# Kernel tuning notes

Measured on AMD Instinct MI355X. Metric: run time of the kernel, lower is better.

## Reference

```python
import jax, jax.numpy as jnp
import numpy as np

B, N = 32, 262144

def setup_inputs() -> dict:
    key = jax.random.key(0)
    k1, k2, k3, k4, k5 = jax.random.split(key, 5)
    F_mat = jax.random.normal(k1, (B, 3, 3), jnp.float32)
    f = 800.0 + 50.0 * jax.random.normal(k2, (B,), jnp.float32)
    K = (jnp.zeros((B, 3, 3), jnp.float32)
         .at[:, 0, 0].set(f).at[:, 1, 1].set(f)
         .at[:, 0, 2].set(320.0).at[:, 1, 2].set(240.0)
         .at[:, 2, 2].set(1.0))
    pts1_flat = jax.random.uniform(k3, (N, 2), jnp.float32) * 640.0
    pts2_flat = jax.random.uniform(k4, (N, 2), jnp.float32) * 640.0
    batch_indices = jnp.sort(jax.random.randint(k5, (N,), 0, B))
    return {"F_mat": F_mat, "K": K, "pts1_flat": pts1_flat,
            "pts2_flat": pts2_flat, "batch_indices": batch_indices}

def _pose_candidates(E):
    # torch.svd returns V (not V^T); the original code uses R = U @ W @ V.
    U, S, Vh = jnp.linalg.svd(E)
    U = U * jnp.where(jnp.linalg.det(U) < 0, -1.0, 1.0)[:, None, None]
    Vh = Vh * jnp.where(jnp.linalg.det(Vh) < 0, -1.0, 1.0)[:, None, None]
    V = jnp.swapaxes(Vh, -1, -2)  # = torch's "Vt" variable (which is V)
    W = jnp.array([[0.0, -1.0, 0.0], [1.0, 0.0, 0.0], [0.0, 0.0, 1.0]], E.dtype)
    R1 = U @ W @ V
    R2 = U @ W.T @ V
    t = U[:, :, 2]
    R_cand = jnp.stack([R1, R1, R2, R2], axis=1)          # [B,4,3,3]
    t_cand = jnp.stack([t, -t, t, -t], axis=1)            # [B,4,3]
    return R_cand, t_cand

def _cheirality_scores(R_cand, t_cand, K, pts1_flat, pts2_flat, batch_indices):
    n = pts1_flat.shape[0]
    Kinv = jnp.linalg.inv(K)[batch_indices]               # [N,3,3]
    ones = jnp.ones((n, 1), pts1_flat.dtype)
    p1 = jnp.einsum('nij,nj->ni', Kinv, jnp.concatenate([pts1_flat, ones], 1))[:, :2]
    p2 = jnp.einsum('nij,nj->ni', Kinv, jnp.concatenate([pts2_flat, ones], 1))[:, :2]
    P2 = jnp.concatenate([R_cand, t_cand[..., None]], axis=-1)  # [B,4,3,4]
    P2n = P2[batch_indices]                                     # [N,4,3,4]
    # A rows for P1 = [I|0]: A0 = [-1,0,x1,0], A1 = [0,-1,y1,0]
    z = jnp.zeros((n,), p1.dtype)
    A0 = jnp.stack([-jnp.ones_like(z), z, p1[:, 0], z], axis=-1)  # [N,4]
    A1 = jnp.stack([z, -jnp.ones_like(z), p1[:, 1], z], axis=-1)
    A2 = p2[:, 0, None, None] * P2n[:, :, 2, :] - P2n[:, :, 0, :]  # [N,4,4]
    A3 = p2[:, 1, None, None] * P2n[:, :, 2, :] - P2n[:, :, 1, :]
    A = jnp.stack([jnp.broadcast_to(A0[:, None, :], A2.shape),
                   jnp.broadcast_to(A1[:, None, :], A2.shape), A2, A3], axis=2)  # [N,4,4,4]
    _, _, Vh = jnp.linalg.svd(A)
    vec = Vh[..., :, -1]                      # = last ROW of V, faithful to torch code
    pts3d = vec[..., :3] / vec[..., 3:4]      # [N,4,3]
    z1 = pts3d[..., 2]                        # depth in cam 1 (P1 = [I|0])
    z2 = jnp.sum(P2n[:, :, 2, :3] * pts3d, axis=-1) + P2n[:, :, 2, 3]
    in_front = ((z1 > 0) & (z2 > 0)).astype(jnp.float32)  # [N,4]
    scores = jax.ops.segment_sum(in_front, batch_indices, num_segments=B)  # [B,4]
    counts = jax.ops.segment_sum(jnp.ones((n,), jnp.float32), batch_indices, num_segments=B)
    return scores, counts

def reference(F_mat, K, pts1_flat, pts2_flat, batch_indices):
    E = jnp.einsum('bji,bjk,bkl->bil', K, F_mat, K)       # K^T F K
    R_cand, t_cand = _pose_candidates(E)
    scores, counts = _cheirality_scores(R_cand, t_cand, K, pts1_flat, pts2_flat, batch_indices)
    best_idx = jnp.argmax(scores, axis=1)                 # first max, like torch '>'
    has = (counts > 0).astype(R_cand.dtype)
    bi = jnp.arange(B)
    best_R = R_cand[bi, best_idx] * has[:, None, None]
    best_t = t_cand[bi, best_idx] * has[:, None]
    best_candidate = jnp.where(counts > 0, best_idx, 0)
    return best_R, best_t, best_candidate
```

## Files before the change

### kernel.cpp

```cpp
#include <hip/hip_runtime.h>
#include <math.h>


#define NBATCH 32
#define USE_NEW_SLARTG 1

#define EPS4  5.9604645e-08f
#define UNFL4 1.1754944e-38f
#define TOL4  (10.0f * EPS4)


__device__ __forceinline__ float sign_f(float a, float b) {
  return (b >= 0.0f) ? fabsf(a) : -fabsf(a);
}

__device__ __forceinline__ float slapy2f(float x, float y) {
#pragma clang fp contract(off)
  float xa = fabsf(x), ya = fabsf(y);
  float w = fmaxf(xa, ya), z = fminf(xa, ya);
  if (z == 0.0f) return w;
  float r = z / w;
  return w * sqrtf(1.0f + r * r);
}

__device__ __forceinline__ void slartg_(float f, float g, float* cs, float* sn, float* r) {
#pragma clang fp contract(off)
#if USE_NEW_SLARTG
  if (g == 0.0f) { *cs = 1.0f; *sn = 0.0f; *r = f; return; }
  if (f == 0.0f) { *cs = 0.0f; *sn = (g >= 0.0f) ? 1.0f : -1.0f; *r = fabsf(g); return; }
  float d = sqrtf(f * f + g * g);
  *cs = fabsf(f) / d;
  float rr = (f >= 0.0f) ? d : -d;
  *sn = g / rr;
  *r = rr;
#else
  if (g == 0.0f) { *cs = 1.0f; *sn = 0.0f; *r = f; return; }
  if (f == 0.0f) { *cs = 0.0f; *sn = 1.0f; *r = g; return; }
  float rr = sqrtf(f * f + g * g);
  float c = f / rr, s = g / rr;
  if (fabsf(f) > fabsf(g) && c < 0.0f) { c = -c; s = -s; rr = -rr; }
  *cs = c; *sn = s; *r = rr;
#endif
}

__device__ __forceinline__ void slas2_(float f, float g, float h, float* ssmin, float* ssmax) {
#pragma clang fp contract(off)
  float fa = fabsf(f), ga = fabsf(g), ha = fabsf(h);
  float fhmn = fminf(fa, ha), fhmx = fmaxf(fa, ha);
  if (fhmn == 0.0f) {
    *ssmin = 0.0f;
    if (fhmx == 0.0f) { *ssmax = ga; }
    else {
      float mx = fmaxf(fhmx, ga), mn = fminf(fhmx, ga);
      float r = mn / mx;
      *ssmax = mx * sqrtf(1.0f + r * r);
    }
  } else {
    if (ga < fhmx) {
      float as_ = 1.0f + fhmn / fhmx;
      float at = (fhmx - fhmn) / fhmx;
      float au = ga / fhmx; au = au * au;
      float c = 2.0f / (sqrtf(as_ * as_ + au) + sqrtf(at * at + au));
      *ssmin = fhmn * c;
      *ssmax = fhmx / c;
    } else {
      float au = fhmx / ga;
      if (au == 0.0f) { *ssmin = (fhmn * fhmx) / ga; *ssmax = ga; }
      else {
        float as_ = 1.0f + fhmn / fhmx;
        float at = (fhmx - fhmn) / fhmx;
        float aas = as_ * au, aat = at * au;
        float c = 1.0f / (sqrtf(1.0f + aas * aas) + sqrtf(1.0f + aat * aat));
        float sm = (fhmn * c) * au;
        *ssmin = sm + sm;
        *ssmax = ga / (c + c);
      }
    }
  }
}

__device__ __forceinline__ void slasv2_(float f, float g, float h, float* ssmin, float* ssmax,
                        float* snr, float* csr, float* snl, float* csl) {
#pragma clang fp contract(off)
  const float EPS = EPS4;
  float ft = f, fa = fabsf(f), ht = h, ha = fabsf(h);
  int pmax = 1;
  bool swap_ = (ha > fa);
  if (swap_) {
    pmax = 3;
    float t = ft; ft = ht; ht = t;
    t = fa; fa = ha; ha = t;
  }
  float gt = g, ga = fabsf(g);
  float clt = 0.f, crt = 0.f, slt = 0.f, srt = 0.f;
  if (ga == 0.0f) {
    *ssmin = ha; *ssmax = fa;
    clt = 1.0f; crt = 1.0f; slt = 0.0f; srt = 0.0f;
  } else {
    bool gasmal = true;
    if (ga > fa) {
      pmax = 2;
      if ((fa / ga) < EPS) {
        gasmal = false;
        *ssmax = ga;
        if (ha > 1.0f) *ssmin = fa / (ga / ha);
        else *ssmin = (fa / ga) * ha;
        clt = 1.0f; slt = ht / gt; srt = 1.0f; crt = ft / gt;
      }
    }
    if (gasmal) {
      float dd = fa - ha;
      float l;
      if (dd == fa) l = 1.0f; else l = dd / fa;
      float mm_ = gt / ft;
      float t = 2.0f - l;
      float mm = mm_ * mm_, tt = t * t;
      float s = sqrtf(tt + mm);
      float r;
      if (l == 0.0f) r = fabsf(mm_); else r = sqrtf(l * l + mm);
      float a = 0.5f * (s + r);
      *ssmin = ha / a;
      *ssmax = fa * a;
      if (mm == 0.0f) {
        if (l == 0.0f) t = sign_f(2.0f, ft) * sign_f(1.0f, gt);
        else t = gt / sign_f(dd, ft) + mm_ / t;
      } else {
        t = (mm_ / (s + t) + mm_ / (r + l)) * (1.0f + a);
      }
      float l2 = sqrtf(t * t + 4.0f);
      crt = 2.0f / l2;
      srt = t / l2;
      clt = (crt + srt * mm_) / a;
      slt = (ht / ft) * srt / a;
    }
  }
  if (swap_) { *csl = srt; *snl = crt; *csr = slt; *snr = clt; }
  else { *csl = clt; *snl = slt; *csr = crt; *snr = srt; }
  float tsign = 1.0f;
  if (pmax == 1) tsign = sign_f(1.0f, *csr) * sign_f(1.0f, *csl) * sign_f(1.0f, f);
  if (pmax == 2) tsign = sign_f(1.0f, *snr) * sign_f(1.0f, *csl) * sign_f(1.0f, g);
  if (pmax == 3) tsign = sign_f(1.0f, *snr) * sign_f(1.0f, *snl) * sign_f(1.0f, h);
  *ssmax = sign_f(*ssmax, tsign);
  *ssmin = sign_f(*ssmin, tsign * sign_f(1.0f, f) * sign_f(1.0f, h));
}


__device__ __forceinline__ void sv3_chase(float (&d)[3], float (&e)[2],
                                          float (&vt)[3][3], float (&u)[3][3],
                                          float thresh, int& iter, int& oldll,
                                          int& oldm, int& idir, float smax) {
#pragma clang fp contract(off)
  if (1 > oldm || 3 < oldll)
    idir = (fabsf(d[0]) >= fabsf(d[2])) ? 1 : 2;

  bool deflated = false;
  float sminl = 0.0f;
  if (idir == 1) {
    if (fabsf(e[1]) <= TOL4 * fabsf(d[2])) { e[1] = 0.0f; return; }
    float mu = fabsf(d[0]); sminl = mu;
    if (fabsf(e[0]) <= TOL4 * mu) { e[0] = 0.0f; deflated = true; }
    else {
      mu = fabsf(d[1]) * (mu / (mu + fabsf(e[0])));
      if (mu < sminl) sminl = mu;
      if (fabsf(e[1]) <= TOL4 * mu) { e[1] = 0.0f; deflated = true; }
      else {
        mu = fabsf(d[2]) * (mu / (mu + fabsf(e[1])));
        if (mu < sminl) sminl = mu;
      }
    }
  } else {
    if (fabsf(e[0]) <= TOL4 * fabsf(d[0])) { e[0] = 0.0f; return; }
    float mu = fabsf(d[2]); sminl = mu;
    if (fabsf(e[1]) <= TOL4 * mu) { e[1] = 0.0f; deflated = true; }
    else {
      mu = fabsf(d[1]) * (mu / (mu + fabsf(e[1])));
      if (mu < sminl) sminl = mu;
      if (fabsf(e[0]) <= TOL4 * mu) { e[0] = 0.0f; deflated = true; }
      else {
        mu = fabsf(d[0]) * (mu / (mu + fabsf(e[0])));
        if (mu < sminl) sminl = mu;
      }
    }
  }
  if (deflated) return;
  oldll = 1; oldm = 3;

  float shift = 0.0f, rdum;
  if (!(3.0f * TOL4 * (sminl / smax) <= fmaxf(EPS4, 0.01f * TOL4))) {
    float sll;
    if (idir == 1) { sll = fabsf(d[0]); slas2_(d[1], e[1], d[2], &shift, &rdum); }
    else { sll = fabsf(d[2]); slas2_(d[0], e[0], d[1], &shift, &rdum); }
    if (sll > 0.0f) {
      float q = shift / sll;
      if (q * q < EPS4) shift = 0.0f;
    }
  }
  iter += 2;

  if (shift == 0.0f) {
    if (idir == 1) {
      float cs = 1.0f, oldcs = 1.0f, sn = 0.0f, oldsn = 0.0f, r = 0.0f;
      float c1, s1, c2, s2, rr;
      slartg_(d[0] * cs, e[0], &c1, &s1, &r); cs = c1; sn = s1;
      slartg_(oldcs * r, d[1] * sn, &c2, &s2, &rr); oldcs = c2; oldsn = s2;
      d[0] = rr;
#pragma unroll
      for (int k = 0; k < 3; k++) {
        float x = vt[0][k], y = vt[1][k];
        vt[0][k] = cs * x + sn * y; vt[1][k] = cs * y - sn * x;
      }
#pragma unroll
      for (int k = 0; k < 3; k++) {
        float x = u[k][0], y = u[k][1];
        u[k][0] = oldcs * x + oldsn * y; u[k][1] = oldcs * y - oldsn * x;
      }
      slartg_(d[1] * cs, e[1], &c1, &s1, &r); cs = c1; sn = s1;
      e[0] = oldsn * r;
      slartg_(oldcs * r, d[2] * sn, &c2, &s2, &rr); oldcs = c2; oldsn = s2;
      d[1] = rr;
#pragma unroll
      for (int k = 0; k < 3; k++) {
        float x = vt[1][k], y = vt[2][k];
        vt[1][k] = cs * x + sn * y; vt[2][k] = cs * y - sn * x;
      }
#pragma unroll
      for (int k = 0; k < 3; k++) {
        float x = u[k][1], y = u[k][2];
        u[k][1] = oldcs * x + oldsn * y; u[k][2] = oldcs * y - oldsn * x;
      }
      float h = d[2] * cs;
      d[2] = h * oldcs;
      e[1] = h * oldsn;
      if (fabsf(e[1]) <= thresh) e[1] = 0.0f;
    } else {
      float cs = 1.0f, oldcs = 1.0f, sn = 0.0f, oldsn = 0.0f, r = 0.0f;
      float c1, s1, c2, s2, rr;
      slartg_(d[2] * cs, e[1], &c1, &s1, &r); cs = c1; sn = s1;
      slartg_(oldcs * r, d[1] * sn, &c2, &s2, &rr); oldcs = c2; oldsn = s2;
      d[2] = rr;
#pragma unroll
      for (int k = 0; k < 3; k++) {
        float x = u[k][2], y = u[k][1];
        u[k][2] = cs * x + sn * y; u[k][1] = cs * y - sn * x;
      }
#pragma unroll
      for (int k = 0; k < 3; k++) {
        float x = vt[2][k], y = vt[1][k];
        vt[2][k] = oldcs * x + oldsn * y; vt[1][k] = oldcs * y - oldsn * x;
      }
      slartg_(d[1] * cs, e[0], &c1, &s1, &r); cs = c1; sn = s1;
      e[1] = oldsn * r;
      slartg_(oldcs * r, d[0] * sn, &c2, &s2, &rr); oldcs = c2; oldsn = s2;
      d[1] = rr;
#pragma unroll
      for (int k = 0; k < 3; k++) {
        float x = u[k][1], y = u[k][0];
        u[k][1] = cs * x + sn * y; u[k][0] = cs * y - sn * x;
      }
#pragma unroll
      for (int k = 0; k < 3; k++) {
        float x = vt[1][k], y = vt[0][k];
        vt[1][k] = oldcs * x + oldsn * y; vt[0][k] = oldcs * y - oldsn * x;
      }
      float h = d[0] * cs;
      d[0] = h * oldcs;
      e[0] = h * oldsn;
      if (fabsf(e[0]) <= thresh) e[0] = 0.0f;
    }
  } else {
    if (idir == 1) {
      float f = (fabsf(d[0]) - shift) * (sign_f(1.0f, d[0]) + shift / d[0]);
      float g = e[0];
      float cosr, sinr, cosl, sinl, r, rr;
      slartg_(f, g, &cosr, &sinr, &r);
      f = cosr * d[0] + sinr * e[0];
      e[0] = cosr * e[0] - sinr * d[0];
      g = sinr * d[1];
      d[1] = cosr * d[1];
      slartg_(f, g, &cosl, &sinl, &rr);
      d[0] = rr;
      f = cosl * e[0] + sinl * d[1];
      d[1] = cosl * d[1] - sinl * e[0];
      g = sinl * e[1];
      e[1] = cosl * e[1];
#pragma unroll
      for (int k = 0; k < 3; k++) {
        float x = vt[0][k], y = vt[1][k];
        vt[0][k] = cosr * x + sinr * y; vt[1][k] = cosr * y - sinr * x;
      }
#pragma unroll
      for (int k = 0; k < 3; k++) {
        float x = u[k][0], y = u[k][1];
        u[k][0] = cosl * x + sinl * y; u[k][1] = cosl * y - sinl * x;
      }
      slartg_(f, g, &cosr, &sinr, &r);
      e[0] = r;
      f = cosr * d[1] + sinr * e[1];
      e[1] = cosr * e[1] - sinr * d[1];
      g = sinr * d[2];
      d[2] = cosr * d[2];
      slartg_(f, g, &cosl, &sinl, &rr);
      d[1] = rr;
      f = cosl * e[1] + sinl * d[2];
      d[2] = cosl * d[2] - sinl * e[1];
#pragma unroll
      for (int k = 0; k < 3; k++) {
        float x = vt[1][k], y = vt[2][k];
        vt[1][k] = cosr * x + sinr * y; vt[2][k] = cosr * y - sinr * x;
      }
#pragma unroll
      for (int k = 0; k < 3; k++) {
        float x = u[k][1], y = u[k][2];
        u[k][1] = cosl * x + sinl * y; u[k][2] = cosl * y - sinl * x;
      }
      e[1] = f;
      if (fabsf(e[1]) <= thresh) e[1] = 0.0f;
    } else {
      float f = (fabsf(d[2]) - shift) * (sign_f(1.0f, d[2]) + shift / d[2]);
      float g = e[1];
      float cosr, sinr, cosl, sinl, r, rr;
      slartg_(f, g, &cosr, &sinr, &r);
      f = cosr * d[2] + sinr * e[1];
      e[1] = cosr * e[1] - sinr * d[2];
      g = sinr * d[1];
      d[1] = cosr * d[1];
      slartg_(f, g, &cosl, &sinl, &rr);
      d[2] = rr;
      f = cosl * e[1] + sinl * d[1];
      d[1] = cosl * d[1] - sinl * e[1];
      g = sinl * e[0];
      e[0] = cosl * e[0];
#pragma unroll
      for (int k = 0; k < 3; k++) {
        float x = u[k][2], y = u[k][1];
        u[k][2] = cosr * x + sinr * y; u[k][1] = cosr * y - sinr * x;
      }
#pragma unroll
      for (int k = 0; k < 3; k++) {
        float x = vt[2][k], y = vt[1][k];
        vt[2][k] = cosl * x + sinl * y; vt[1][k] = cosl * y - sinl * x;
      }
      slartg_(f, g, &cosr, &sinr, &r);
      e[1] = r;
      f = cosr * d[1] + sinr * e[0];
      e[0] = cosr * e[0] - sinr * d[1];
      g = sinr * d[0];
      d[0] = cosr * d[0];
      slartg_(f, g, &cosl, &sinl, &rr);
      d[1] = rr;
      f = cosl * e[0] + sinl * d[0];
      d[0] = cosl * d[0] - sinl * e[0];
#pragma unroll
      for (int k = 0; k < 3; k++) {
        float x = u[k][1], y = u[k][0];
        u[k][1] = cosr * x + sinr * y; u[k][0] = cosr * y - sinr * x;
      }
#pragma unroll
      for (int k = 0; k < 3; k++) {
        float x = vt[1][k], y = vt[0][k];
        vt[1][k] = cosl * x + sinl * y; vt[0][k] = cosl * y - sinl * x;
      }
      e[0] = f;
      if (fabsf(e[0]) <= thresh) e[0] = 0.0f;
    }
  }
}

__device__ __forceinline__ void sv3_iter3(float (&d)[3], float (&e)[2],
                                          float (&vt)[3][3], float (&u)[3][3],
                                          float thresh, int& m, int& iter,
                                          int& oldll, int& oldm, int& idir) {
#pragma clang fp contract(off)
  float smax = fabsf(d[2]);
  int ll = 0;
  bool split = false;
  if (fabsf(e[1]) <= thresh) { split = true; ll = 2; }
  else {
    smax = fmaxf(smax, fmaxf(fabsf(d[1]), fabsf(e[1])));
    if (fabsf(e[0]) <= thresh) { split = true; ll = 1; }
    else {
      smax = fmaxf(smax, fmaxf(fabsf(d[0]), fabsf(e[0])));
      ll = 1;
    }
  }
  if (split) {
    if (ll == 2) { e[1] = 0.0f; m = 2; return; }
    e[0] = 0.0f;
    float sigmn, sigmx, sinr, cosr, sinl, cosl;
    slasv2_(d[1], e[1], d[2], &sigmn, &sigmx, &sinr, &cosr, &sinl, &cosl);
    d[1] = sigmx; e[1] = 0.0f; d[2] = sigmn;
#pragma unroll
    for (int k = 0; k < 3; k++) {
      float x = vt[1][k], y = vt[2][k];
      vt[1][k] = cosr * x + sinr * y; vt[2][k] = cosr * y - sinr * x;
    }
#pragma unroll
    for (int k = 0; k < 3; k++) {
      float x = u[k][1], y = u[k][2];
      u[k][1] = cosl * x + sinl * y; u[k][2] = cosl * y - sinl * x;
    }
    m = 1;
    return;
  }
  sv3_chase(d, e, vt, u, thresh, iter, oldll, oldm, idir, smax);
}

__device__ __forceinline__ void sv3_iter2(float (&d)[3], float (&e)[2],
                                          float (&vt)[3][3], float (&u)[3][3],
                                          float thresh, int& m) {
#pragma clang fp contract(off)
  if (fabsf(e[0]) <= thresh) { e[0] = 0.0f; m = 1; return; }
  float sigmn, sigmx, sinr, cosr, sinl, cosl;
  slasv2_(d[0], e[0], d[1], &sigmn, &sigmx, &sinr, &cosr, &sinl, &cosl);
  d[0] = sigmx; e[0] = 0.0f; d[1] = sigmn;
#pragma unroll
  for (int k = 0; k < 3; k++) {
    float x = vt[0][k], y = vt[1][k];
    vt[0][k] = cosr * x + sinr * y; vt[1][k] = cosr * y - sinr * x;
  }
#pragma unroll
  for (int k = 0; k < 3; k++) {
    float x = u[k][0], y = u[k][1];
    u[k][0] = cosl * x + sinl * y; u[k][1] = cosl * y - sinl * x;
  }
  m = 0;
}

__device__ void gesdd3_pose(const float E[9], float (&u)[3][3], float (&vt)[3][3]) {
#pragma clang fp contract(off)
  float a[3][3];
#pragma unroll
  for (int i = 0; i < 3; i++)
#pragma unroll
    for (int j = 0; j < 3; j++) a[i][j] = E[i * 3 + j];
  float d[3], e[2], tauq[3], taup[2];

  {
    float alpha = a[0][0];
    float ss = a[1][0] * a[1][0] + a[2][0] * a[2][0];
    if (ss == 0.0f) { tauq[0] = 0.0f; d[0] = alpha; }
    else {
      float xnorm = sqrtf(ss);
      float beta = -sign_f(slapy2f(alpha, xnorm), alpha);
      tauq[0] = (beta - alpha) / beta;
      float scal = 1.0f / (alpha - beta);
      a[1][0] *= scal; a[2][0] *= scal;
      d[0] = beta;
    }
#pragma unroll
    for (int c = 1; c < 3; c++) {
      float w = (a[0][c] + a[1][0] * a[1][c]) + a[2][0] * a[2][c];
      float tw = tauq[0] * w;
      a[0][c] -= tw; a[1][c] -= tw * a[1][0]; a[2][c] -= tw * a[2][0];
    }
    float alpha2 = a[0][1];
    float ss2 = a[0][2] * a[0][2];
    if (ss2 == 0.0f) { taup[0] = 0.0f; e[0] = alpha2; }
    else {
      float xnorm = sqrtf(ss2);
      float beta = -sign_f(slapy2f(alpha2, xnorm), alpha2);
      taup[0] = (beta - alpha2) / beta;
      float scal = 1.0f / (alpha2 - beta);
      a[0][2] *= scal;
      e[0] = beta;
    }
#pragma unroll
    for (int r = 1; r < 3; r++) {
      float w = a[r][1] + a[r][2] * a[0][2];
      float tw = taup[0] * w;
      a[r][1] -= tw; a[r][2] -= tw * a[0][2];
    }
  }
  {
    float alpha = a[1][1];
    float ss = a[2][1] * a[2][1];
    if (ss == 0.0f) { tauq[1] = 0.0f; d[1] = alpha; }
    else {
      float xnorm = sqrtf(ss);
      float beta = -sign_f(slapy2f(alpha, xnorm), alpha);
      tauq[1] = (beta - alpha) / beta;
      float scal = 1.0f / (alpha - beta);
      a[2][1] *= scal;
      d[1] = beta;
    }
    {
      float w = a[1][2] + a[2][1] * a[2][2];
      float tw = tauq[1] * w;
      a[1][2] -= tw; a[2][2] -= tw * a[2][1];
    }
    taup[1] = 0.0f; e[1] = a[1][2];
    {
      float w = a[2][2];
      float tw = taup[1] * w;
      a[2][2] -= tw;
    }
  }
  tauq[2] = 0.0f;
  d[2] = a[2][2];

#pragma unroll
  for (int i = 0; i < 3; i++)
#pragma unroll
    for (int j = 0; j < 3; j++) {
      vt[i][j] = (i == j) ? 1.0f : 0.0f;
      u[i][j] = (i == j) ? 1.0f : 0.0f;
    }

  {
    float sminoa = fabsf(d[0]);
    if (sminoa != 0.0f) {
      float mu = sminoa;
      mu = fabsf(d[1]) * (mu / (mu + fabsf(e[0])));
      if (mu < sminoa) sminoa = mu;
      if (sminoa != 0.0f) {
        mu = fabsf(d[2]) * (mu / (mu + fabsf(e[1])));
        if (mu < sminoa) sminoa = mu;
      }
    }
    sminoa = sminoa / sqrtf(3.0f);
    float thresh = fmaxf(TOL4 * sminoa, 54.0f * UNFL4);
    int m = 3, iter = 0, oldll = -1, oldm = -1, idir = 0, guard = 0;
    while (guard++ < 500) {
      if (m <= 1 || iter > 54) break;
      if (m == 3) sv3_iter3(d, e, vt, u, thresh, m, iter, oldll, oldm, idir);
      else sv3_iter2(d, e, vt, u, thresh, m);
    }
  }

#pragma unroll
  for (int i = 0; i < 3; i++) {
    if (d[i] < 0.0f) {
      d[i] = -d[i];
#pragma unroll
      for (int k = 0; k < 3; k++) vt[i][k] = -vt[i][k];
    }
  }
  {
    int isub = 1; float smn = d[0];
    if (d[1] <= smn) { isub = 2; smn = d[1]; }
    if (d[2] <= smn) { isub = 3; smn = d[2]; }
    if (isub != 3) {
      if (isub == 1) {
        d[0] = d[2];
#pragma unroll
        for (int k = 0; k < 3; k++) { float t = vt[0][k]; vt[0][k] = vt[2][k]; vt[2][k] = t; }
#pragma unroll
        for (int k = 0; k < 3; k++) { float t = u[k][0]; u[k][0] = u[k][2]; u[k][2] = t; }
      } else {
        d[1] = d[2];
#pragma unroll
        for (int k = 0; k < 3; k++) { float t = vt[1][k]; vt[1][k] = vt[2][k]; vt[2][k] = t; }
#pragma unroll
        for (int k = 0; k < 3; k++) { float t = u[k][1]; u[k][1] = u[k][2]; u[k][2] = t; }
      }
      d[2] = smn;
    }
  }
  {
    int isub = 1; float smn = d[0];
    if (d[1] <= smn) { isub = 2; smn = d[1]; }
    if (isub != 2) {
      d[0] = d[1]; d[1] = smn;
#pragma unroll
      for (int k = 0; k < 3; k++) { float t = vt[0][k]; vt[0][k] = vt[1][k]; vt[1][k] = t; }
#pragma unroll
      for (int k = 0; k < 3; k++) { float t = u[k][0]; u[k][0] = u[k][1]; u[k][1] = t; }
    }
  }

#pragma unroll
  for (int c = 0; c < 3; c++) {
    float w = u[2][c];
    float tw = tauq[2] * w;
    u[2][c] -= tw;
  }
#pragma unroll
  for (int c = 0; c < 3; c++) {
    float w = u[1][c] + a[2][1] * u[2][c];
    float tw = tauq[1] * w;
    u[1][c] -= tw; u[2][c] -= tw * a[2][1];
  }
#pragma unroll
  for (int c = 0; c < 3; c++) {
    float w = (u[0][c] + a[1][0] * u[1][c]) + a[2][0] * u[2][c];
    float tw = tauq[0] * w;
    u[0][c] -= tw; u[1][c] -= tw * a[1][0]; u[2][c] -= tw * a[2][0];
  }
#pragma unroll
  for (int r = 0; r < 3; r++) {
    float w = vt[r][2];
    float tw = taup[1] * w;
    vt[r][2] -= tw;
  }
#pragma unroll
  for (int r = 0; r < 3; r++) {
    float w = vt[r][1] + vt[r][2] * a[0][2];
    float tw = taup[0] * w;
    vt[r][1] -= tw; vt[r][2] -= tw * a[0][2];
  }
}

__device__ __forceinline__ float det3f(const float M[3][3]) {
#pragma clang fp contract(off)
  return M[0][0] * (M[1][1] * M[2][2] - M[1][2] * M[2][1])
       - M[0][1] * (M[1][0] * M[2][2] - M[1][2] * M[2][0])
       + M[0][2] * (M[1][0] * M[2][1] - M[1][1] * M[2][0]);
}


template <int LL, int M>
__device__ __forceinline__ void sv_rev(float (&d)[4], float (&e)[3], float (&vt)[4][4]) {
#pragma unroll
  for (int k = 0; k < (M - LL + 1) / 2; k++) {
    float t = d[LL - 1 + k]; d[LL - 1 + k] = d[M - 1 - k]; d[M - 1 - k] = t;
  }
#pragma unroll
  for (int k = 0; k < (M - LL) / 2; k++) {
    float t = e[LL - 1 + k]; e[LL - 1 + k] = e[M - 2 - k]; e[M - 2 - k] = t;
  }
#pragma unroll
  for (int k = 0; k < (M - LL + 1) / 2; k++)
#pragma unroll
    for (int c = 1; c < 4; c++) {
      float t = vt[LL - 1 + k][c]; vt[LL - 1 + k][c] = vt[M - 1 - k][c]; vt[M - 1 - k][c] = t;
    }
}

template <int LL, int M>
__device__ __forceinline__ void sv_chase_m(float (&d)[4], float (&e)[3], float (&vt)[4][4],
                                           float thresh, int& iter, int& oldll, int& oldm,
                                           int& idir, float smax) {
#pragma clang fp contract(off)
  if (LL > oldm || M < oldll)
    idir = (fabsf(d[LL - 1]) >= fabsf(d[M - 1])) ? 1 : 2;
  const bool rev = (idir == 2);

  if (rev) sv_rev<LL, M>(d, e, vt);

  bool done = false;
  if (fabsf(e[M - 2]) <= TOL4 * fabsf(d[M - 1])) { e[M - 2] = 0.0f; done = true; }

  float sminl = 0.0f;
  if (!done) {
    float mu = fabsf(d[LL - 1]); sminl = mu;
    bool defl = false;
#pragma unroll
    for (int lll = LL; lll <= M - 1; lll++) {
      if (!defl) {
        if (fabsf(e[lll - 1]) <= TOL4 * mu) { e[lll - 1] = 0.0f; defl = true; }
        else {
          mu = fabsf(d[lll]) * (mu / (mu + fabsf(e[lll - 1])));
          if (mu < sminl) sminl = mu;
        }
      }
    }
    if (defl) done = true;
  }

  if (!done) {
    oldll = LL; oldm = M;

    float shift = 0.0f, rdum;
    if (!(4.0f * TOL4 * (sminl / smax) <= fmaxf(EPS4, 0.01f * TOL4))) {
      float sll = fabsf(d[LL - 1]);
      slas2_(d[M - 2], e[M - 2], d[M - 1], &shift, &rdum);
      if (sll > 0.0f) {
        float q = shift / sll;
        if (q * q < EPS4) shift = 0.0f;
      }
    }
    iter += M - LL;

    if (shift == 0.0f) {
      float cs = 1.0f, oldcs = 1.0f, sn = 0.0f, oldsn = 0.0f, r = 0.0f;
#pragma unroll
      for (int i = LL; i <= M - 1; i++) {
        float c1, s1;
        slartg_(d[i - 1] * cs, e[i - 1], &c1, &s1, &r);
        cs = c1; sn = s1;
        if (i > LL) e[i - 2] = oldsn * r;
        float c2, s2, rr;
        slartg_(oldcs * r, d[i] * sn, &c2, &s2, &rr);
        oldcs = c2; oldsn = s2;
        d[i - 1] = rr;
        float cu = rev ? oldcs : cs;
        float su = rev ? oldsn : sn;
#pragma unroll
        for (int k = 1; k < 4; k++) {
          float x = vt[i - 1][k], y = vt[i][k];
          vt[i - 1][k] = cu * x + su * y; vt[i][k] = cu * y - su * x;
        }
      }
      float h = d[M - 1] * cs;
      d[M - 1] = h * oldcs;
      e[M - 2] = h * oldsn;
      if (fabsf(e[M - 2]) <= thresh) e[M - 2] = 0.0f;
    } else {
      float f = (fabsf(d[LL - 1]) - shift) * (sign_f(1.0f, d[LL - 1]) + shift / d[LL - 1]);
      float g = e[LL - 1];
#pragma unroll
      for (int i = LL; i <= M - 1; i++) {
        float cosr, sinr, r;
        slartg_(f, g, &cosr, &sinr, &r);
        if (i > LL) e[i - 2] = r;
        f = cosr * d[i - 1] + sinr * e[i - 1];
        e[i - 1] = cosr * e[i - 1] - sinr * d[i - 1];
        g = sinr * d[i];
        d[i] = cosr * d[i];
        float cosl, sinl, rr;
        slartg_(f, g, &cosl, &sinl, &rr);
        d[i - 1] = rr;
        f = cosl * e[i - 1] + sinl * d[i];
        d[i] = cosl * d[i] - sinl * e[i - 1];
        if (i < M - 1) {
          g = sinl * e[i];
          e[i] = cosl * e[i];
        }
        float cu = rev ? cosl : cosr;
        float su = rev ? sinl : sinr;
#pragma unroll
        for (int k = 1; k < 4; k++) {
          float x = vt[i - 1][k], y = vt[i][k];
          vt[i - 1][k] = cu * x + su * y; vt[i][k] = cu * y - su * x;
        }
      }
      e[M - 2] = f;
      if (fabsf(e[M - 2]) <= thresh) e[M - 2] = 0.0f;
    }
  }

  if (rev) sv_rev<LL, M>(d, e, vt);
}

template <int M>
__device__ __forceinline__ void sv_iter(float (&d)[4], float (&e)[3], float (&vt)[4][4],
                                        float thresh, int& m, int& iter,
                                        int& oldll, int& oldm, int& idir) {
#pragma clang fp contract(off)
  float smax = fabsf(d[M - 1]);
  float smin = smax;
  int ll = 0;
  bool split = false;
#pragma unroll
  for (int lll = 1; lll <= M - 1; lll++) {
    if (!split) {
      const int llc = M - lll;
      float abss = fabsf(d[llc - 1]);
      float abse = fabsf(e[llc - 1]);
      if (abse <= thresh) { split = true; ll = llc; }
      else {
        if (abss < smin) smin = abss;
        float mx = fmaxf(abss, abse);
        if (mx > smax) smax = mx;
        ll = llc;
      }
    }
  }
  (void)smin;
  if (split) {
    if (ll == 1) e[0] = 0.0f;
    else if (M > 2 && ll == 2) e[1] = 0.0f;
    else if (M > 3) e[2] = 0.0f;
    if (ll == M - 1) { m = M - 1; return; }
    ll = ll + 1;
  } else {
    ll = 1;
  }
  if (ll == M - 1) {
    float sigmn, sigmx, sinr, cosr, sinl, cosl;
    slasv2_(d[M - 2], e[M - 2], d[M - 1], &sigmn, &sigmx, &sinr, &cosr, &sinl, &cosl);
    d[M - 2] = sigmx; e[M - 2] = 0.0f; d[M - 1] = sigmn;
#pragma unroll
    for (int k = 1; k < 4; k++) {
      float x = vt[M - 2][k], y = vt[M - 1][k];
      vt[M - 2][k] = cosr * x + sinr * y; vt[M - 1][k] = cosr * y - sinr * x;
    }
    m = M - 2;
    return;
  }
  if constexpr (M == 4) {
    if (ll == 2) sv_chase_m<2, 4>(d, e, vt, thresh, iter, oldll, oldm, idir, smax);
    else sv_chase_m<1, 4>(d, e, vt, thresh, iter, oldll, oldm, idir, smax);
  } else if constexpr (M == 3) {
    sv_chase_m<1, 3>(d, e, vt, thresh, iter, oldll, oldm, idir, smax);
  }
}

__device__ __forceinline__ void gesdd4_vec(const float A0[16], float vec[4]) {
#pragma clang fp contract(off)
  float a[4][4];
#pragma unroll
  for (int i = 0; i < 4; i++)
#pragma unroll
    for (int j = 0; j < 4; j++) a[i][j] = A0[i * 4 + j];
  float d[4], e[3], tauq[4], taup[3];

#pragma unroll
  for (int i = 0; i < 4; i++) {
    float alpha = a[i][i];
    float ss = 0.0f;
#pragma unroll
    for (int r = i + 1; r < 4; r++) ss += a[r][i] * a[r][i];
    if (ss == 0.0f) { tauq[i] = 0.0f; d[i] = alpha; }
    else {
      float xnorm = sqrtf(ss);
      float beta = -sign_f(slapy2f(alpha, xnorm), alpha);
      tauq[i] = (beta - alpha) / beta;
      float scal = 1.0f / (alpha - beta);
#pragma unroll
      for (int r = i + 1; r < 4; r++) a[r][i] *= scal;
      d[i] = beta;
    }
#pragma unroll
    for (int c = i + 1; c < 4; c++) {
      float w = a[i][c];
#pragma unroll
      for (int r = i + 1; r < 4; r++) w += a[r][i] * a[r][c];
      float tw = tauq[i] * w;
      a[i][c] -= tw;
#pragma unroll
      for (int r = i + 1; r < 4; r++) a[r][c] -= tw * a[r][i];
    }
    if (i < 3) {
      float alpha2 = a[i][i + 1];
      float ss2 = 0.0f;
#pragma unroll
      for (int c = i + 2; c < 4; c++) ss2 += a[i][c] * a[i][c];
      if (ss2 == 0.0f) { taup[i] = 0.0f; e[i] = alpha2; }
      else {
        float xnorm = sqrtf(ss2);
        float beta = -sign_f(slapy2f(alpha2, xnorm), alpha2);
        taup[i] = (beta - alpha2) / beta;
        float scal = 1.0f / (alpha2 - beta);
#pragma unroll
        for (int c = i + 2; c < 4; c++) a[i][c] *= scal;
        e[i] = beta;
      }
#pragma unroll
      for (int r = i + 1; r < 4; r++) {
        float w = a[r][i + 1];
#pragma unroll
        for (int c = i + 2; c < 4; c++) w += a[r][c] * a[i][c];
        float tw = taup[i] * w;
        a[r][i + 1] -= tw;
#pragma unroll
        for (int c = i + 2; c < 4; c++) a[r][c] -= tw * a[i][c];
      }
    }
  }

  float vt[4][4];
#pragma unroll
  for (int i = 0; i < 4; i++)
#pragma unroll
    for (int k = 1; k < 4; k++) vt[i][k] = (i == k) ? 1.0f : 0.0f;

  float sminoa = fabsf(d[0]);
  if (sminoa != 0.0f) {
    float mu = sminoa;
    bool zr = false;
#pragma unroll
    for (int i = 2; i <= 4; i++) {
      if (!zr) {
        mu = fabsf(d[i - 1]) * (mu / (mu + fabsf(e[i - 2])));
        if (mu < sminoa) sminoa = mu;
        if (sminoa == 0.0f) zr = true;
      }
    }
  }
  sminoa = sminoa / sqrtf(4.0f);
  float thresh = fmaxf(TOL4 * sminoa, 96.0f * UNFL4);
  const int maxit = 96;

  int m = 4, iter = 0, oldll = -1, oldm = -1, idir = 0;
  for (int g = 0; g < 300; g++) {
    bool act = (m == 4) && (iter <= maxit);
    if (!__any(act)) break;
    if (act) sv_iter<4>(d, e, vt, thresh, m, iter, oldll, oldm, idir);
  }
  for (int g = 0; g < 300; g++) {
    bool act = (m == 3) && (iter <= maxit);
    if (!__any(act)) break;
    if (act) sv_iter<3>(d, e, vt, thresh, m, iter, oldll, oldm, idir);
  }
  for (int g = 0; g < 300; g++) {
    bool act = (m == 2) && (iter <= maxit);
    if (!__any(act)) break;
    if (act) sv_iter<2>(d, e, vt, thresh, m, iter, oldll, oldm, idir);
  }

#pragma unroll
  for (int i = 0; i < 4; i++) {
    if (d[i] < 0.0f) {
      d[i] = -d[i];
#pragma unroll
      for (int k = 1; k < 4; k++) vt[i][k] = -vt[i][k];
    }
  }
  {
    int isub = 1; float smn = d[0];
    if (d[1] <= smn) { isub = 2; smn = d[1]; }
    if (d[2] <= smn) { isub = 3; smn = d[2]; }
    if (d[3] <= smn) { isub = 4; smn = d[3]; }
    if (isub != 4) {
      if (isub == 1) {
        d[0] = d[3];
#pragma unroll
        for (int k = 1; k < 4; k++) { float t = vt[0][k]; vt[0][k] = vt[3][k]; vt[3][k] = t; }
      } else if (isub == 2) {
        d[1] = d[3];
#pragma unroll
        for (int k = 1; k < 4; k++) { float t = vt[1][k]; vt[1][k] = vt[3][k]; vt[3][k] = t; }
      } else {
        d[2] = d[3];
#pragma unroll
        for (int k = 1; k < 4; k++) { float t = vt[2][k]; vt[2][k] = vt[3][k]; vt[3][k] = t; }
      }
      d[3] = smn;
    }
  }
  {
    int isub = 1; float smn = d[0];
    if (d[1] <= smn) { isub = 2; smn = d[1]; }
    if (d[2] <= smn) { isub = 3; smn = d[2]; }
    if (isub != 3) {
      if (isub == 1) {
        d[0] = d[2];
#pragma unroll
        for (int k = 1; k < 4; k++) { float t = vt[0][k]; vt[0][k] = vt[2][k]; vt[2][k] = t; }
      } else {
        d[1] = d[2];
#pragma unroll
        for (int k = 1; k < 4; k++) { float t = vt[1][k]; vt[1][k] = vt[2][k]; vt[2][k] = t; }
      }
      d[2] = smn;
    }
  }
  {
    int isub = 1; float smn = d[0];
    if (d[1] <= smn) { isub = 2; smn = d[1]; }
    if (isub != 2) {
      d[0] = d[1];
#pragma unroll
      for (int k = 1; k < 4; k++) { float t = vt[0][k]; vt[0][k] = vt[1][k]; vt[1][k] = t; }
      d[1] = smn;
    }
  }

#pragma unroll
  for (int r = 0; r < 4; r++) {
    float w = vt[r][2] + vt[r][3] * a[1][3];
    float tw = taup[1] * w;
    vt[r][2] -= tw;
    vt[r][3] -= tw * a[1][3];
  }
#pragma unroll
  for (int r = 0; r < 4; r++) {
    float w = (vt[r][1] + vt[r][2] * a[0][2]) + vt[r][3] * a[0][3];
    float tw = taup[0] * w;
    vt[r][1] -= tw;
    vt[r][2] -= tw * a[0][2];
    vt[r][3] -= tw * a[0][3];
  }

  vec[0] = vt[0][3]; vec[1] = vt[1][3]; vec[2] = vt[2][3]; vec[3] = vt[3][3];
}


__global__ __launch_bounds__(64) void pose_kernel(const float* __restrict__ Fm,
                                                  const float* __restrict__ Km,
                                                  float* __restrict__ ws) {
  int b = blockIdx.x;
  if (threadIdx.x != 0 || b >= NBATCH) return;
  float* wsR = ws;
  float* wsT = ws + 1152;
  float* wsK = ws + 1536;
  int* scores = (int*)(ws + 1664);
  int* counts = (int*)(ws + 1792);
  for (int c = 0; c < 4; c++) scores[b * 4 + c] = 0;
  counts[b] = 0;
  {
#pragma clang fp contract(off)
    const float* F = Fm + b * 9;
    const float* K = Km + b * 9;
    float E[9];
    for (int i = 0; i < 3; i++) for (int l = 0; l < 3; l++) {
      float acc = 0.0f;
      for (int j = 0; j < 3; j++)
        for (int k = 0; k < 3; k++)
          acc += (K[j * 3 + i] * F[j * 3 + k]) * K[k * 3 + l];
      E[i * 3 + l] = acc;
    }
    float U[3][3], VT[3][3];
    gesdd3_pose(E, U, VT);
    float su = (det3f(U) < 0.0f) ? -1.0f : 1.0f;
    float sv = (det3f(VT) < 0.0f) ? -1.0f : 1.0f;
    for (int i = 0; i < 3; i++) for (int j = 0; j < 3; j++) { U[i][j] *= su; VT[i][j] *= sv; }
    float R1[3][3], R2[3][3];
    for (int r = 0; r < 3; r++) {
      float uw0 = U[r][1], uw1 = -U[r][0], uw2 = U[r][2];
      float vw0 = -U[r][1], vw1 = U[r][0];
      for (int c = 0; c < 3; c++) {
        R1[r][c] = (uw0 * VT[c][0] + uw1 * VT[c][1]) + uw2 * VT[c][2];
        R2[r][c] = (vw0 * VT[c][0] + vw1 * VT[c][1]) + uw2 * VT[c][2];
      }
    }
    float t0 = U[0][2], t1 = U[1][2], t2 = U[2][2];
    for (int c = 0; c < 4; c++) {
      const float (*R)[3] = (c < 2) ? R1 : R2;
      float sg = (c & 1) ? -1.0f : 1.0f;
      float* dst = wsR + (b * 4 + c) * 9;
      for (int i = 0; i < 3; i++) for (int j = 0; j < 3; j++) dst[i * 3 + j] = R[i][j];
      float* dt = wsT + (b * 4 + c) * 3;
      dt[0] = sg * t0; dt[1] = sg * t1; dt[2] = sg * t2;
    }
    const float fx = K[0], fy = K[4], cx = K[2], cy = K[5];
    float invfx = 1.0f / fx, invfy = 1.0f / fy;
    wsK[b * 4 + 0] = invfx;
    wsK[b * 4 + 1] = -(invfx * cx);
    wsK[b * 4 + 2] = invfy;
    wsK[b * 4 + 3] = -(invfy * cy);
  }
}


__global__ __launch_bounds__(256) void score_kernel(const float* __restrict__ pts1,
                                                    const float* __restrict__ pts2,
                                                    const int* __restrict__ bidx,
                                                    float* __restrict__ ws,
                                                    int n_pts) {
  __shared__ float sR[1152];
  __shared__ float sT[384];
  __shared__ float sK[128];
  __shared__ int h01[32], h23[32], hc[32];
  int tid = threadIdx.x;
  for (int i = tid; i < 1152; i += 256) sR[i] = ws[i];
  for (int i = tid; i < 384; i += 256) sT[i] = ws[1152 + i];
  for (int i = tid; i < 128; i += 256) sK[i] = ws[1536 + i];
  if (tid < 32) { h01[tid] = 0; h23[tid] = 0; hc[tid] = 0; }
  __syncthreads();

  int gid = blockIdx.x * 256 + tid;
  int n = gid >> 1, pr = gid & 1;
  bool active = (n < n_pts);
  bool f0 = false, f1 = false;
  int b = 0;
  if (active) {
    b = bidx[n];
    float x1 = pts1[2 * n], y1 = pts1[2 * n + 1];
    float x2 = pts2[2 * n], y2 = pts2[2 * n + 1];
    float invfx = sK[b * 4 + 0], k02 = sK[b * 4 + 1];
    float invfy = sK[b * 4 + 2], k12 = sK[b * 4 + 3];
    const float* R = sR + (b * 4 + 2 * pr) * 9;
    const float* t = sT + (b * 4 + 2 * pr) * 3;
    float Am[16];
    float row2[4] = { R[6], R[7], R[8], t[2] };
    {
#pragma clang fp contract(off)
      float p1x = invfx * x1 + k02;
      float p1y = invfy * y1 + k12;
      float p2x = invfx * x2 + k02;
      float p2y = invfy * y2 + k12;
      float row0[4] = { R[0], R[1], R[2], t[0] };
      float row1[4] = { R[3], R[4], R[5], t[1] };
      Am[0] = -1.0f; Am[1] = 0.0f; Am[2] = p1x; Am[3] = 0.0f;
      Am[4] = 0.0f; Am[5] = -1.0f; Am[6] = p1y; Am[7] = 0.0f;
#pragma unroll
      for (int k = 0; k < 4; k++) {
        Am[8 + k] = p2x * row2[k] - row0[k];
        Am[12 + k] = p2y * row2[k] - row1[k];
      }
    }
    float vec[4];
    gesdd4_vec(Am, vec);
    {
#pragma clang fp contract(off)
      float v3 = vec[3];
      float X = vec[0] / v3, Y = vec[1] / v3, Z = vec[2] / v3;
      float p0 = row2[0] * X, p1 = row2[1] * Y, p2 = row2[2] * Z;
      float s = (p0 + p1) + p2;
      float t2 = row2[3];
      float z2a = s + t2;
      float z2b = s + (-t2);
      bool zpos = (Z > 0.0f);
      f0 = zpos && (z2a > 0.0f);
      f1 = zpos && (z2b > 0.0f);
    }
  }
  if (active) {
    int add = (f0 ? 1 : 0) | (f1 ? (1 << 16) : 0);
    if (add) {
      if (pr == 0) atomicAdd(&h01[b], add);
      else atomicAdd(&h23[b], add);
    }
    if (pr == 0) atomicAdd(&hc[b], 1);
  }
  __syncthreads();
  if (tid < 32) {
    int* scores = (int*)(ws + 1664);
    int* counts = (int*)(ws + 1792);
    int v01 = h01[tid], v23 = h23[tid], vc = hc[tid];
    if (v01 & 0xFFFF) atomicAdd(&scores[tid * 4 + 0], v01 & 0xFFFF);
    if (v01 >> 16) atomicAdd(&scores[tid * 4 + 1], v01 >> 16);
    if (v23 & 0xFFFF) atomicAdd(&scores[tid * 4 + 2], v23 & 0xFFFF);
    if (v23 >> 16) atomicAdd(&scores[tid * 4 + 3], v23 >> 16);
    if (vc) atomicAdd(&counts[tid], vc);
  }
}


__global__ __launch_bounds__(64) void final_kernel(const float* __restrict__ ws,
                                                   float* __restrict__ out) {
  int b = threadIdx.x;
  if (b >= NBATCH) return;
  const int* scores = (const int*)(ws + 1664);
  const int* counts = (const int*)(ws + 1792);
  int best = 0, bs = scores[b * 4];
  for (int c = 1; c < 4; c++) {
    int sc = scores[b * 4 + c];
    if (sc > bs) { bs = sc; best = c; }
  }
  int cnt = counts[b];
  float has = (cnt > 0) ? 1.0f : 0.0f;
  const float* R = ws + (b * 4 + best) * 9;
  const float* t = ws + 1152 + (b * 4 + best) * 3;
  for (int k = 0; k < 9; k++) out[b * 9 + k] = R[k] * has;
  for (int k = 0; k < 3; k++) out[288 + b * 3 + k] = t[k] * has;
  out[384 + b] = (cnt > 0) ? (float)best : 0.0f;
}


extern "C" void kernel_launch(void* const* d_in, const int* in_sizes, int n_in,
                              void* d_out, int out_size, void* d_ws, size_t ws_size,
                              hipStream_t stream) {
  (void)n_in; (void)out_size; (void)ws_size;
  const float* F = (const float*)d_in[0];
  const float* K = (const float*)d_in[1];
  const float* p1 = (const float*)d_in[2];
  const float* p2 = (const float*)d_in[3];
  const int* bi = (const int*)d_in[4];
  int n_pts = in_sizes[4];
  float* ws = (float*)d_ws;
  float* out = (float*)d_out;

  pose_kernel<<<NBATCH, 64, 0, stream>>>(F, K, ws);
  int total = n_pts * 2;
  int blocks = (total + 255) / 256;
  score_kernel<<<blocks, 256, 0, stream>>>(p1, p2, bi, ws, n_pts);
  final_kernel<<<1, 64, 0, stream>>>(ws, out);
}
```

Before: 190.3 us.

## Fuse pose, scoring and final selection into one kernel with last-block reduction

Measured after the change: 201.4 us. 5.8% more time.

```diff
diff --git a/kernel.cpp b/kernel.cpp
--- a/kernel.cpp
+++ b/kernel.cpp
@@ -967,77 +967,67 @@
 }
 
 
-__global__ __launch_bounds__(64) void pose_kernel(const float* __restrict__ Fm,
-                                                  const float* __restrict__ Km,
-                                                  float* __restrict__ ws) {
-  int b = blockIdx.x;
-  if (threadIdx.x != 0 || b >= NBATCH) return;
-  float* wsR = ws;
-  float* wsT = ws + 1152;
-  float* wsK = ws + 1536;
-  int* scores = (int*)(ws + 1664);
-  int* counts = (int*)(ws + 1792);
-  for (int c = 0; c < 4; c++) scores[b * 4 + c] = 0;
-  counts[b] = 0;
-  {
-#pragma clang fp contract(off)
-    const float* F = Fm + b * 9;
-    const float* K = Km + b * 9;
-    float E[9];
-    for (int i = 0; i < 3; i++) for (int l = 0; l < 3; l++) {
-      float acc = 0.0f;
-      for (int j = 0; j < 3; j++)
-        for (int k = 0; k < 3; k++)
-          acc += (K[j * 3 + i] * F[j * 3 + k]) * K[k * 3 + l];
-      E[i * 3 + l] = acc;
-    }
-    float U[3][3], VT[3][3];
-    gesdd3_pose(E, U, VT);
-    float su = (det3f(U) < 0.0f) ? -1.0f : 1.0f;
-    float sv = (det3f(VT) < 0.0f) ? -1.0f : 1.0f;
-    for (int i = 0; i < 3; i++) for (int j = 0; j < 3; j++) { U[i][j] *= su; VT[i][j] *= sv; }
-    float R1[3][3], R2[3][3];
-    for (int r = 0; r < 3; r++) {
-      float uw0 = U[r][1], uw1 = -U[r][0], uw2 = U[r][2];
-      float vw0 = -U[r][1], vw1 = U[r][0];
-      for (int c = 0; c < 3; c++) {
-        R1[r][c] = (uw0 * VT[c][0] + uw1 * VT[c][1]) + uw2 * VT[c][2];
-        R2[r][c] = (vw0 * VT[c][0] + vw1 * VT[c][1]) + uw2 * VT[c][2];
-      }
-    }
-    float t0 = U[0][2], t1 = U[1][2], t2 = U[2][2];
-    for (int c = 0; c < 4; c++) {
-      const float (*R)[3] = (c < 2) ? R1 : R2;
-      float sg = (c & 1) ? -1.0f : 1.0f;
-      float* dst = wsR + (b * 4 + c) * 9;
-      for (int i = 0; i < 3; i++) for (int j = 0; j < 3; j++) dst[i * 3 + j] = R[i][j];
-      float* dt = wsT + (b * 4 + c) * 3;
-      dt[0] = sg * t0; dt[1] = sg * t1; dt[2] = sg * t2;
-    }
-    const float fx = K[0], fy = K[4], cx = K[2], cy = K[5];
-    float invfx = 1.0f / fx, invfy = 1.0f / fy;
-    wsK[b * 4 + 0] = invfx;
-    wsK[b * 4 + 1] = -(invfx * cx);
-    wsK[b * 4 + 2] = invfy;
-    wsK[b * 4 + 3] = -(invfy * cy);
-  }
-}
-
-
-__global__ __launch_bounds__(256) void score_kernel(const float* __restrict__ pts1,
+__global__ __launch_bounds__(256) void fused_kernel(const float* __restrict__ Fm,
+                                                    const float* __restrict__ Km,
+                                                    const float* __restrict__ pts1,
                                                     const float* __restrict__ pts2,
                                                     const int* __restrict__ bidx,
                                                     float* __restrict__ ws,
+                                                    float* __restrict__ out,
                                                     int n_pts) {
   __shared__ float sR[1152];
   __shared__ float sT[384];
   __shared__ float sK[128];
   __shared__ int h01[32], h23[32], hc[32];
+  __shared__ int lastFlag;
   int tid = threadIdx.x;
-  for (int i = tid; i < 1152; i += 256) sR[i] = ws[i];
-  for (int i = tid; i < 384; i += 256) sT[i] = ws[1152 + i];
-  for (int i = tid; i < 128; i += 256) sK[i] = ws[1536 + i];
-  if (tid < 32) { h01[tid] = 0; h23[tid] = 0; hc[tid] = 0; }
+
+  if (tid < 32) {
+    int b = tid;
+    h01[b] = 0; h23[b] = 0; hc[b] = 0;
+    {
+#pragma clang fp contract(off)
+      const float* F = Fm + b * 9;
+      const float* K = Km + b * 9;
+      float E[9];
+      for (int i = 0; i < 3; i++) for (int l = 0; l < 3; l++) {
+        float acc = 0.0f;
+        for (int j = 0; j < 3; j++)
+          for (int k = 0; k < 3; k++)
+            acc += (K[j * 3 + i] * F[j * 3 + k]) * K[k * 3 + l];
+        E[i * 3 + l] = acc;
+      }
+      float U[3][3], VT[3][3];
+      gesdd3_pose(E, U, VT);
+      float su = (det3f(U) < 0.0f) ? -1.0f : 1.0f;
+      float sv = (det3f(VT) < 0.0f) ? -1.0f : 1.0f;
+      for (int i = 0; i < 3; i++) for (int j = 0; j < 3; j++) { U[i][j] *= su; VT[i][j] *= sv; }
+      float R1[3][3], R2[3][3];
+      for (int r = 0; r < 3; r++) {
+        float uw0 = U[r][1], uw1 = -U[r][0], uw2 = U[r][2];
+        float vw0 = -U[r][1], vw1 = U[r][0];
+        for (int c = 0; c < 3; c++) {
+          R1[r][c] = (uw0 * VT[c][0] + uw1 * VT[c][1]) + uw2 * VT[c][2];
+          R2[r][c] = (vw0 * VT[c][0] + vw1 * VT[c][1]) + uw2 * VT[c][2];
+        }
+      }
+      float t0 = U[0][2], t1 = U[1][2], t2 = U[2][2];
+      for (int c = 0; c < 4; c++) {
+        const float (*R)[3] = (c < 2) ? R1 : R2;
+        float sg = (c & 1) ? -1.0f : 1.0f;
+        float* dst = sR + (b * 4 + c) * 9;
+        for (int i = 0; i < 3; i++) for (int j = 0; j < 3; j++) dst[i * 3 + j] = R[i][j];
+        float* dt = sT + (b * 4 + c) * 3;
+        dt[0] = sg * t0; dt[1] = sg * t1; dt[2] = sg * t2;
+      }
+      const float fx = K[0], fy = K[4], cx = K[2], cy = K[5];
+      float invfx = 1.0f / fx, invfy = 1.0f / fy;
+      sK[b * 4 + 0] = invfx;
+      sK[b * 4 + 1] = -(invfx * cx);
+      sK[b * 4 + 2] = invfy;
+      sK[b * 4 + 3] = -(invfy * cy);
+    }
+  }
   __syncthreads();
 
   int gid = blockIdx.x * 256 + tid;
@@ -1096,9 +1086,11 @@
     if (pr == 0) atomicAdd(&hc[b], 1);
   }
   __syncthreads();
+
+  int* scores = (int*)ws + 1664;
+  int* counts = (int*)ws + 1792;
+  int* counter = (int*)ws + 1824;
   if (tid < 32) {
-    int* scores = (int*)(ws + 1664);
-    int* counts = (int*)(ws + 1792);
     int v01 = h01[tid], v23 = h23[tid], vc = hc[tid];
     if (v01 & 0xFFFF) atomicAdd(&scores[tid * 4 + 0], v01 & 0xFFFF);
     if (v01 >> 16) atomicAdd(&scores[tid * 4 + 1], v01 >> 16);
@@ -1106,27 +1098,32 @@
     if (v23 >> 16) atomicAdd(&scores[tid * 4 + 3], v23 >> 16);
     if (vc) atomicAdd(&counts[tid], vc);
   }
-}
-
-
-__global__ __launch_bounds__(64) void final_kernel(const float* __restrict__ ws,
-                                                   float* __restrict__ out) {
-  int b = threadIdx.x;
-  if (b >= NBATCH) return;
-  const int* scores = (const int*)(ws + 1664);
-  const int* counts = (const int*)(ws + 1792);
-  int best = 0, bs = scores[b * 4];
-  for (int c = 1; c < 4; c++) {
-    int sc = scores[b * 4 + c];
-    if (sc > bs) { bs = sc; best = c; }
-  }
-  int cnt = counts[b];
-  float has = (cnt > 0) ? 1.0f : 0.0f;
-  const float* R = ws + (b * 4 + best) * 9;
-  const float* t = ws + 1152 + (b * 4 + best) * 3;
-  for (int k = 0; k < 9; k++) out[b * 9 + k] = R[k] * has;
-  for (int k = 0; k < 3; k++) out[288 + b * 3 + k] = t[k] * has;
-  out[384 + b] = (cnt > 0) ? (float)best : 0.0f;
+  __syncthreads();
+
+  if (tid == 0) {
+    __threadfence();
+    int old = atomicAdd(counter, 1);
+    lastFlag = (old == (int)gridDim.x - 1) ? 1 : 0;
+  }
+  __syncthreads();
+  if (lastFlag && tid < 32) {
+    int bb = tid;
+    int s0 = atomicAdd(&scores[bb * 4 + 0], 0);
+    int s1 = atomicAdd(&scores[bb * 4 + 1], 0);
+    int s2 = atomicAdd(&scores[bb * 4 + 2], 0);
+    int s3 = atomicAdd(&scores[bb * 4 + 3], 0);
+    int cnt = atomicAdd(&counts[bb], 0);
+    int best = 0, bs = s0;
+    if (s1 > bs) { bs = s1; best = 1; }
+    if (s2 > bs) { bs = s2; best = 2; }
+    if (s3 > bs) { bs = s3; best = 3; }
+    float has = (cnt > 0) ? 1.0f : 0.0f;
+    const float* R = sR + (bb * 4 + best) * 9;
+    const float* t = sT + (bb * 4 + best) * 3;
+    for (int k = 0; k < 9; k++) out[bb * 9 + k] = R[k] * has;
+    for (int k = 0; k < 3; k++) out[288 + bb * 3 + k] = t[k] * has;
+    out[384 + bb] = (cnt > 0) ? (float)best : 0.0f;
+  }
 }
 
 
@@ -1143,9 +1140,9 @@
   float* ws = (float*)d_ws;
   float* out = (float*)d_out;
 
-  pose_kernel<<<NBATCH, 64, 0, stream>>>(F, K, ws);
+  (void)hipMemsetAsync((char*)d_ws + 1664 * 4, 0, (1825 - 1664) * 4, stream);
+
   int total = n_pts * 2;
   int blocks = (total + 255) / 256;
-  score_kernel<<<blocks, 256, 0, stream>>>(p1, p2, bi, ws, n_pts);
-  final_kernel<<<1, 64, 0, stream>>>(ws, out);
-}
+  fused_kernel<<<blocks, 256, 0, stream>>>(F, K, p1, p2, bi, ws, out, n_pts);
+}
```
